# Kernel optimization log

Hardware: AMD Instinct MI355X
Metric: run time of the kernel (lower is better)

The kernel has to match this reference:

```python
import jax, jax.numpy as jnp
import numpy as np

# Model dims (match init_kwargs)
B, N, FIN, C, D, L, H = 16, 64, 16, 32, 4, 4, 8
EPS = 1e-6


def _sph(rhat):
    """Real spherical harmonics Y_l(rhat) for l=0..3. rhat: [...,3] unit vectors."""
    x, y, z = rhat[..., 0], rhat[..., 1], rhat[..., 2]
    Y0 = jnp.full(rhat.shape[:-1] + (1,), 0.5 * np.sqrt(1.0 / np.pi), rhat.dtype)
    c1 = np.sqrt(3.0 / (4.0 * np.pi))
    Y1 = c1 * jnp.stack([y, z, x], axis=-1)
    Y2 = jnp.stack([
        0.5 * np.sqrt(15 / np.pi) * x * y,
        0.5 * np.sqrt(15 / np.pi) * y * z,
        0.25 * np.sqrt(5 / np.pi) * (3 * z * z - 1.0),
        0.5 * np.sqrt(15 / np.pi) * x * z,
        0.25 * np.sqrt(15 / np.pi) * (x * x - y * y)], axis=-1)
    Y3 = jnp.stack([
        0.25 * np.sqrt(35 / (2 * np.pi)) * y * (3 * x * x - y * y),
        0.5 * np.sqrt(105 / np.pi) * x * y * z,
        0.25 * np.sqrt(21 / (2 * np.pi)) * y * (5 * z * z - 1.0),
        0.25 * np.sqrt(7 / np.pi) * z * (5 * z * z - 3.0),
        0.25 * np.sqrt(21 / (2 * np.pi)) * x * (5 * z * z - 1.0),
        0.25 * np.sqrt(105 / np.pi) * z * (x * x - y * y),
        0.25 * np.sqrt(35 / (2 * np.pi)) * x * (x * x - y * y)], axis=-1)
    return [Y0, Y1, Y2, Y3]


def _ln(v):
    mu = v.mean(-1, keepdims=True)
    var = ((v - mu) ** 2).mean(-1, keepdims=True)
    return (v - mu) * jax.lax.rsqrt(var + EPS)


def _forward(h, x, bond_type, Wemb, rw1, rb1, rw2, rb2, Wk, Wv, Wq, Wself, gnorm, bnorm, Wfinal, bfinal):
    Bq, Nq, _ = h.shape
    hd = C // H  # channels per head
    # Fully-connected graph: rel_pos[b, dst, src] = x_src - x_dst (matches xi[src]-xi[dst])
    rel = x[:, None, :, :] - x[:, :, None, :]
    dist = jnp.sqrt((rel * rel).sum(-1) + EPS)  # [B,N,N]
    rhat = rel / dist[..., None]
    Ys = _sph(rhat)
    # bond types -> one-hot(5) dropping class 0 -> 4 edge channels
    ef = jax.nn.one_hot(jnp.clip(bond_type, 0, 4), 5, dtype=h.dtype)[..., 1:]
    rin = jnp.concatenate([dist[..., None], ef], axis=-1)  # [B,N,N,5]
    eye = jnp.eye(Nq, dtype=bool)[None, :, :, None]  # mask self-edges
    # embed node feats to num_channels type-0; higher degrees start at zero
    f = [jnp.einsum('bnf,fc->bnc', h, Wemb)[..., None]] + \
        [jnp.zeros((Bq, Nq, C, 2 * l + 1), h.dtype) for l in range(1, D)]
    scale = 1.0 / np.sqrt(hd * sum(2 * l + 1 for l in range(D)))
    for li in range(L):
        # radial MLP with layer norm on (dist, edge_feat)
        hmid = jax.nn.relu(_ln(jnp.einsum('bdsi,ic->bdsc', rin, rw1[li]) + rb1[li]))
        r = (jnp.einsum('bdsc,co->bdso', hmid, rw2[li]) + rb2[li]).reshape(Bq, Nq, Nq, D, 4, C)
        logits = jnp.zeros((Bq, Nq, Nq, H), h.dtype)
        vs = []
        f0 = f[0][..., 0]  # [B,N,C]
        for l in range(D):
            M = 2 * l + 1
            # equivariant paths: (0->l) via Y_l lift, (l->l) identity
            sc_k = jnp.einsum('ci,bni->bnc', Wk[li, l, 0], f0)
            sc_v = jnp.einsum('ci,bni->bnc', Wv[li, l, 0], f0)
            id_k = jnp.einsum('ci,bnim->bncm', Wk[li, l, 1], f[l])
            id_v = jnp.einsum('ci,bnim->bncm', Wv[li, l, 1], f[l])
            Yl = Ys[l][:, :, :, None, :]  # [B,N,N,1,M]
            k = r[..., l, 0, :, None] * sc_k[:, None, :, :, None] * Yl + r[..., l, 1, :, None] * id_k[:, None]
            v = r[..., l, 2, :, None] * sc_v[:, None, :, :, None] * Yl + r[..., l, 3, :, None] * id_v[:, None]
            q = jnp.einsum('ci,bnim->bncm', Wq[li, l], f[l])  # dst-side query
            logits = logits + jnp.einsum('bdhcm,bdshcm->bdsh',
                                         q.reshape(Bq, Nq, H, hd, M),
                                         k.reshape(Bq, Nq, Nq, H, hd, M))
            vs.append(v)
        logits = jnp.where(eye, -1e9, logits * scale)
        attn = jax.nn.softmax(logits, axis=2)  # softmax over source nodes
        newf = []
        for l in range(D):
            M = 2 * l + 1
            o = jnp.einsum('bdsh,bdshcm->bdhcm', attn,
                           vs[l].reshape(Bq, Nq, Nq, H, hd, M)).reshape(Bq, Nq, C, M)
            o = o + jnp.einsum('ci,bnim->bncm', Wself[li, l], f[l])  # self-interaction skip
            # NormSE3: per-channel norm over the 2l+1 components, gated nonlinearity
            nrm = jnp.sqrt((o * o).sum(-1) + EPS)
            s = jax.nn.relu(gnorm[li, l] * nrm + bnorm[li, l])
            newf.append(o * (s / nrm)[..., None])
        f = newf
    # invariant readout: fiber_out = {0: D*C}; proj is Identity since D*C == d_gnn == 128
    inv = jnp.concatenate([f[0][..., 0]] + [jnp.sqrt((f[l] ** 2).sum(-1) + EPS) for l in range(1, D)], axis=-1)
    node_out = inv @ Wfinal + bfinal  # [B,N,128]
    return node_out.mean(axis=1)  # avg pooling -> [B,128]


def setup_inputs() -> dict:
    key = jax.random.key(0)
    ks = jax.random.split(key, 12)
    h = jax.random.normal(ks[0], (B, N, FIN), jnp.float32)
    x = 2.0 * jax.random.normal(ks[1], (B, N, 3), jnp.float32)
    bond_type = jax.random.randint(ks[2], (B, N, N), 0, 5)

    def init(k, shape, fan):
        return jax.random.normal(k, shape, jnp.float32) / np.sqrt(fan)

    return {
        'h': h, 'x': x, 'bond_type': bond_type,
        'Wemb': init(ks[3], (FIN, C), FIN),
        'rw1': init(ks[4], (L, 5, C), 5),
        'rb1': jnp.zeros((L, C), jnp.float32),
        'rw2': init(ks[5], (L, C, D * 4 * C), C),
        'rb2': jnp.zeros((L, D * 4 * C), jnp.float32),
        'Wk': init(ks[6], (L, D, 2, C, C), C),
        'Wv': init(ks[7], (L, D, 2, C, C), C),
        'Wq': init(ks[8], (L, D, C, C), C),
        'Wself': init(ks[9], (L, D, C, C), C),
        'gnorm': jnp.ones((L, D, C), jnp.float32),
        'bnorm': jnp.zeros((L, D, C), jnp.float32),
        'Wfinal': init(ks[10], (D * C, 128), D * C),
        'bfinal': jnp.zeros((128,), jnp.float32),
    }


def reference(h, x, bond_type, Wemb, rw1, rb1, rw2, rb2, Wk, Wv, Wq, Wself, gnorm, bnorm, Wfinal, bfinal):
    return _forward(h, x, bond_type, Wemb, rw1, rb1, rw2, rb2, Wk, Wv, Wq, Wself, gnorm, bnorm, Wfinal, bfinal)
```

## Files before the change

kernel.cpp:

```cpp
#include <hip/hip_runtime.h>
#include <hip/hip_bf16.h>


typedef float  f32x4  __attribute__((ext_vector_type(4)));
typedef short  bf16x8 __attribute__((ext_vector_type(8)));

__device__ __forceinline__ int lof(int mg)   { return (mg==0)?0:((mg<4)?1:((mg<9)?2:3)); }
__device__ __forceinline__ int mgb_of(int l) { return (l==0)?0:((l==1)?1:((l==2)?4:9)); }

__device__ __forceinline__ void nf_project2(const float* fl, float* out,
    const float* __restrict__ Wk, const float* __restrict__ Wv,
    const float* __restrict__ Wq, int li, int tid, int nT) {
  for (int o = tid; o < 2560; o += nT) {
    float acc = 0.f;
    if (o < 512) {
      int c = o >> 4, mg = o & 15, l = lof(mg);
      const float* w = Wq + (size_t)((li*4 + l)*32 + c) * 32;
      #pragma unroll
      for (int i = 0; i < 32; i++) acc += w[i] * fl[i*16 + mg];
    } else if (o < 1536) {
      int s = (o - 512) >> 1, kv = (o - 512) & 1;
      int c = s >> 4, mg = s & 15, l = lof(mg);
      const float* w = (kv ? Wv : Wk) + (size_t)(((li*4 + l)*2 + 1)*32 + c) * 32;
      #pragma unroll
      for (int i = 0; i < 32; i++) acc += w[i] * fl[i*16 + mg];
    } else {
      int s = (o - 1536) >> 1, kv = (o - 1536) & 1;
      int c = s >> 4, l = lof(s & 15);
      const float* w = (kv ? Wv : Wk) + (size_t)(((li*4 + l)*2 + 0)*32 + c) * 32;
      #pragma unroll
      for (int i = 0; i < 32; i++) acc += w[i] * fl[i*16];
    }
    out[o] = acc;
  }
}

__global__ __launch_bounds__(256) void prep_k(const float* __restrict__ h,
    const float* __restrict__ Wemb,
    const float* __restrict__ Wk, const float* __restrict__ Wv,
    const float* __restrict__ Wq,
    const float* __restrict__ rw2, const float* __restrict__ rb2,
    float* __restrict__ f, float* __restrict__ nf,
    __hip_bfloat16* __restrict__ rw2bh, __hip_bfloat16* __restrict__ rw2bl,
    float* __restrict__ rb2p) {
  __shared__ __align__(16) float fl[512];
  const int node = blockIdx.x;
  const int tid = threadIdx.x;

  const int gidx = blockIdx.x * 256 + tid;
  if (gidx < 65536) {
    int lli = gidx >> 14, rem = gidx & 16383;
    int np = rem >> 5, k = rem & 31;
    int c = np >> 4, l = (np >> 2) & 3, p = np & 3;
    float v = rw2[(size_t)lli*16384 + k*512 + l*128 + p*32 + c];
    __hip_bfloat16 hi = __float2bfloat16(v);
    __hip_bfloat16 lo = __float2bfloat16(v - __bfloat162float(hi));
    rw2bh[gidx] = hi;
    rw2bl[gidx] = lo;
  }
  if (gidx < 2048) {
    int lli = gidx >> 9, np = gidx & 511;
    int c = np >> 4, l = (np >> 2) & 3, p = np & 3;
    rb2p[gidx] = rb2[lli*512 + l*128 + p*32 + c];
  }

  fl[2*tid] = 0.f; fl[2*tid + 1] = 0.f;
  __syncthreads();
  if (tid < 32) {
    const float* hh = h + node * 16;
    float v = 0.f;
    #pragma unroll
    for (int i = 0; i < 16; i++) v += hh[i] * Wemb[i * 32 + tid];
    fl[tid * 16] = v;
  }
  __syncthreads();
  *reinterpret_cast<float2*>(f + (size_t)node * 512 + 2*tid) =
      *reinterpret_cast<const float2*>(fl + 2*tid);
  nf_project2(fl, nf + (size_t)node * 2560, Wk, Wv, Wq, 0, tid, 256);
}

__global__ __launch_bounds__(256) void attn_k(
    const float* __restrict__ f, const float* __restrict__ nf,
    float* __restrict__ fnext,
    const float* __restrict__ x, const int* __restrict__ bond,
    const float* __restrict__ rw1, const float* __restrict__ rb1,
    const __hip_bfloat16* __restrict__ rw2bh,
    const __hip_bfloat16* __restrict__ rw2bl,
    const float* __restrict__ rb2p,
    const float* __restrict__ Wself, const float* __restrict__ gnorm,
    const float* __restrict__ bnorm,
    const float* __restrict__ Wk, const float* __restrict__ Wv,
    const float* __restrict__ Wq,
    float* __restrict__ nf_out, int li) {
  __shared__ __align__(16) float Ysh[64][16];
  __shared__ float rinsh[64][8];
  __shared__ __align__(16) float fdst[512];
  __shared__ __align__(16) __hip_bfloat16 hmidb_hi[64][40];
  __shared__ __align__(16) __hip_bfloat16 hmidb_lo[64][40];
  __shared__ __align__(16) float rst[4][8*132];

  const int tid = threadIdx.x;
  const int bid = blockIdx.x;
  const int bd  = (bid & 7) * 128 + (bid >> 3);
  const int b = bd >> 6, d = bd & 63;
  const int wv = tid >> 6;
  const int t = tid & 63;

  const int slot0 = 128*wv + 2*t;
  const int oc  = slot0 >> 4;
  const int mg0 = slot0 & 15, mg1 = mg0 + 1;
  const int l0 = lof(mg0), l1 = lof(mg1);

  const int o0 = 2 * tid;
  *reinterpret_cast<float2*>(fdst + o0) =
      *reinterpret_cast<const float2*>(f + (size_t)bd * 512 + o0);
  const float2 qv = *reinterpret_cast<const float2*>(nf + (size_t)bd * 2560 + slot0);

  if (tid < 64) {
    const int s = tid;
    const float* xb = x + (size_t)b * 192;
    float xd = xb[d*3+0], yd = xb[d*3+1], zd = xb[d*3+2];
    float dx = xb[s*3+0] - xd, dy = xb[s*3+1] - yd, dz = xb[s*3+2] - zd;
    float dist = sqrtf(dx*dx + dy*dy + dz*dz + 1e-6f);
    float inv = 1.0f / dist;
    float xx = dx*inv, yy = dy*inv, zz = dz*inv;
    float* Y = Ysh[s];
    Y[0]  = 0.28209479177387814f;
    Y[1]  = 0.4886025119029199f * yy;
    Y[2]  = 0.4886025119029199f * zz;
    Y[3]  = 0.4886025119029199f * xx;
    Y[4]  = 1.0925484305920792f * xx * yy;
    Y[5]  = 1.0925484305920792f * yy * zz;
    Y[6]  = 0.31539156525252005f * (3.0f*zz*zz - 1.0f);
    Y[7]  = 1.0925484305920792f * xx * zz;
    Y[8]  = 0.5462742152960396f * (xx*xx - yy*yy);
    Y[9]  = 0.5900435899266435f * yy * (3.0f*xx*xx - yy*yy);
    Y[10] = 2.890611442640554f  * xx * yy * zz;
    Y[11] = 0.4570457994644658f * yy * (5.0f*zz*zz - 1.0f);
    Y[12] = 0.3731763325901154f * zz * (5.0f*zz*zz - 3.0f);
    Y[13] = 0.4570457994644658f * xx * (5.0f*zz*zz - 1.0f);
    Y[14] = 1.445305721320277f  * zz * (xx*xx - yy*yy);
    Y[15] = 0.5900435899266435f * xx * (xx*xx - yy*yy);
    rinsh[s][0] = dist;
    int bt = bond[(size_t)b * 4096 + d * 64 + s];
    bt = bt < 0 ? 0 : (bt > 4 ? 4 : bt);
    rinsh[s][1] = (bt == 1) ? 1.f : 0.f;
    rinsh[s][2] = (bt == 2) ? 1.f : 0.f;
    rinsh[s][3] = (bt == 3) ? 1.f : 0.f;
    rinsh[s][4] = (bt == 4) ? 1.f : 0.f;
  }

  const int ch = tid & 31;
  float w1r[5];
  #pragma unroll
  for (int i = 0; i < 5; i++) w1r[i] = rw1[(li*5 + i)*32 + ch];
  const float b1r = rb1[li*32 + ch];

  __syncthreads();

  #pragma unroll
  for (int p = 0; p < 8; p++) {
    const int e = p * 8 + (tid >> 5);
    float pre = b1r;
    #pragma unroll
    for (int i = 0; i < 5; i++) pre += rinsh[e][i] * w1r[i];
    float mu = pre;
    #pragma unroll
    for (int k = 16; k >= 1; k >>= 1) mu += __shfl_xor(mu, k, 32);
    mu *= 0.03125f;
    float dv = pre - mu;
    float var = dv * dv;
    #pragma unroll
    for (int k = 16; k >= 1; k >>= 1) var += __shfl_xor(var, k, 32);
    var *= 0.03125f;
    float hm = fmaxf(dv * rsqrtf(var + 1e-6f), 0.0f);
    __hip_bfloat16 hi = __float2bfloat16(hm);
    hmidb_hi[e][ch] = hi;
    hmidb_lo[e][ch] = __float2bfloat16(hm - __bfloat162float(hi));
  }
  __syncthreads();

  const int nfb = (b * 64) * 2560;
  const float4 bA = *reinterpret_cast<const float4*>(rb2p + li*512 + oc*16 + l0*4);
  const float4 bB = *reinterpret_cast<const float4*>(rb2p + li*512 + oc*16 + l1*4);
  const int rdA = (t >> 3)*16 + l0*4;
  const int rdB = (t >> 3)*16 + l1*4;
  const int afoff = li*16384 + (128*wv + (t & 15))*32 + (t >> 4)*8;
  const int bfrow = t & 7;
  const int bfk   = (t >> 4) * 8;
  const int myrow = t & 15;
  const int wcol  = (t >> 4)*4;
  float* rstw = &rst[wv][0];

  float m_run = -1e30f, l_run = 0.0f, acc0 = 0.0f, acc1 = 0.0f;

  auto consume4 = [&](int eg0, int rbase) {
    float4 kvv[4], svv[4];
    #pragma unroll
    for (int e2 = 0; e2 < 4; e2++) {
      const float* npp = nf + nfb + (eg0 + e2) * 2560;
      kvv[e2] = *reinterpret_cast<const float4*>(npp + 512 + 2*slot0);
      svv[e2] = *reinterpret_cast<const float4*>(npp + 1536 + 2*slot0);
    }
    float lg[4], vA[4], vB[4];
    #pragma unroll
    for (int e2 = 0; e2 < 4; e2++) {
      const int eg = eg0 + e2, row = rbase + e2;
      float4 rA = *reinterpret_cast<const float4*>(rstw + row*132 + rdA);
      float4 rB = *reinterpret_cast<const float4*>(rstw + row*132 + rdB);
      rA.x += bA.x; rA.y += bA.y; rA.z += bA.z; rA.w += bA.w;
      rB.x += bB.x; rB.y += bB.y; rB.z += bB.z; rB.w += bB.w;
      const float ym0 = Ysh[eg][mg0], ym1 = Ysh[eg][mg1];
      const float k0 = rA.x * svv[e2].x * ym0 + rA.y * kvv[e2].x;
      const float k1 = rB.x * svv[e2].z * ym1 + rB.y * kvv[e2].z;
      float pl = qv.x * k0 + qv.y * k1;
      pl += __shfl_xor(pl, 1);
      pl += __shfl_xor(pl, 2);
      pl += __shfl_xor(pl, 4);
      pl += __shfl_xor(pl, 8);
      pl += __shfl_xor(pl, 16);
      lg[e2] = (eg == d) ? -1e9f : pl * 0.125f;
      vA[e2] = rA.z * svv[e2].y * ym0 + rA.w * kvv[e2].y;
      vB[e2] = rB.z * svv[e2].w * ym1 + rB.w * kvv[e2].w;
    }
    const float m4 = fmaxf(fmaxf(lg[0], lg[1]), fmaxf(lg[2], lg[3]));
    const float m_new = fmaxf(m_run, m4);
    const float resc = __expf(m_run - m_new);
    acc0 *= resc; acc1 *= resc; l_run *= resc;
    #pragma unroll
    for (int e2 = 0; e2 < 4; e2++) {
      const float wgt = __expf(lg[e2] - m_new);
      l_run += wgt;
      acc0 += wgt * vA[e2];
      acc1 += wgt * vB[e2];
    }
    m_run = m_new;
  };

  for (int mt8 = 0; mt8 < 8; mt8++) {
    const int e0 = mt8 * 8;
    const bf16x8 bhi = *reinterpret_cast<const bf16x8*>(&hmidb_hi[e0 + bfrow][bfk]);
    const bf16x8 blo = *reinterpret_cast<const bf16x8*>(&hmidb_lo[e0 + bfrow][bfk]);
    #pragma unroll
    for (int ct = 0; ct < 8; ct++) {
      const bf16x8 ah = *reinterpret_cast<const bf16x8*>(
          reinterpret_cast<const short*>(rw2bh) + afoff + ct*512);
      const bf16x8 al = *reinterpret_cast<const bf16x8*>(
          reinterpret_cast<const short*>(rw2bl) + afoff + ct*512);
      f32x4 c = {0.f, 0.f, 0.f, 0.f};
      c = __builtin_amdgcn_mfma_f32_16x16x32_bf16(al, bhi, c, 0, 0, 0);
      c = __builtin_amdgcn_mfma_f32_16x16x32_bf16(ah, blo, c, 0, 0, 0);
      c = __builtin_amdgcn_mfma_f32_16x16x32_bf16(ah, bhi, c, 0, 0, 0);
      if (myrow < 8)
        *reinterpret_cast<f32x4*>(rstw + myrow*132 + ct*16 + wcol) = c;
    }
    asm volatile("s_waitcnt lgkmcnt(0)" ::: "memory");
    __builtin_amdgcn_sched_barrier(0);
    consume4(e0,     0);
    consume4(e0 + 4, 4);
  }

  const float invl = 1.0f / l_run;
  acc0 *= invl; acc1 *= invl;
  {
    const float* w0 = Wself + (size_t)((li*4 + l0)*32 + oc) * 32;
    const float* w1 = Wself + (size_t)((li*4 + l1)*32 + oc) * 32;
    #pragma unroll
    for (int i = 0; i < 32; i++) {
      acc0 += w0[i] * fdst[i*16 + mg0];
      acc1 += w1[i] * fdst[i*16 + mg1];
    }
  }
  __syncthreads();
  float* osh = &Ysh[0][0];
  osh[slot0] = acc0; osh[slot0 + 1] = acc1;
  __syncthreads();
  float* facsh = &rinsh[0][0];
  if (tid < 128) {
    const int c2 = tid >> 2, l2 = tid & 3;
    const int mb = mgb_of(l2), M2 = 2*l2 + 1;
    float ss = 0.f;
    for (int m = 0; m < M2; m++) { float v = osh[c2*16 + mb + m]; ss += v*v; }
    const float nrm = sqrtf(ss + 1e-6f);
    const float gg = gnorm[(li*4 + l2)*32 + c2];
    const float bb = bnorm[(li*4 + l2)*32 + c2];
    const float sg = fmaxf(gg*nrm + bb, 0.f);
    facsh[c2*4 + l2] = sg / nrm;
  }
  __syncthreads();
  const float g0 = acc0 * facsh[oc*4 + l0];
  const float g1 = acc1 * facsh[oc*4 + l1];
  *reinterpret_cast<float2*>(fnext + (size_t)bd * 512 + slot0) = make_float2(g0, g1);

  if (nf_out) {
    osh[slot0] = g0; osh[slot0 + 1] = g1;
    __syncthreads();
    nf_project2(osh, nf_out + (size_t)bd * 2560, Wk, Wv, Wq, li + 1, tid, 256);
  }
}

__global__ __launch_bounds__(256) void readout_k(const float* __restrict__ f,
    const float* __restrict__ Wfinal, const float* __restrict__ bfinal,
    float* __restrict__ out) {
  __shared__ float invs[2][128];
  __shared__ float inv1[128];
  const int b = blockIdx.x;
  const int tid = threadIdx.x;
  const int j = tid & 127, half = tid >> 7;
  float p = 0.f;
  for (int n = half*32; n < half*32 + 32; n++) {
    const float* fn = f + (size_t)(b*64 + n) * 512;
    float v;
    if (j < 32) {
      v = fn[j*16];
    } else {
      int l = j >> 5, c = j & 31;
      int mb = mgb_of(l), M = 2*l + 1;
      float ss = 0.f;
      for (int m = 0; m < M; m++) { float t = fn[c*16 + mb + m]; ss += t*t; }
      v = sqrtf(ss + 1e-6f);
    }
    p += v;
  }
  invs[half][j] = p;
  __syncthreads();
  if (tid < 128) inv1[tid] = (invs[0][tid] + invs[1][tid]) * (1.0f / 64.0f);
  __syncthreads();
  if (tid < 128) {
    float acc = bfinal[tid];
    for (int k = 0; k < 128; k++) acc += inv1[k] * Wfinal[k*128 + tid];
    out[b*128 + tid] = acc;
  }
}

extern "C" void kernel_launch(void* const* d_in, const int* in_sizes, int n_in,
                              void* d_out, int out_size, void* d_ws, size_t ws_size,
                              hipStream_t stream) {
  (void)in_sizes; (void)n_in; (void)out_size; (void)ws_size;
  const float* h      = (const float*)d_in[0];
  const float* x      = (const float*)d_in[1];
  const int*   bond   = (const int*)d_in[2];
  const float* Wemb   = (const float*)d_in[3];
  const float* rw1    = (const float*)d_in[4];
  const float* rb1    = (const float*)d_in[5];
  const float* rw2    = (const float*)d_in[6];
  const float* rb2    = (const float*)d_in[7];
  const float* Wk     = (const float*)d_in[8];
  const float* Wv     = (const float*)d_in[9];
  const float* Wq     = (const float*)d_in[10];
  const float* Wself  = (const float*)d_in[11];
  const float* gnorm  = (const float*)d_in[12];
  const float* bnorm  = (const float*)d_in[13];
  const float* Wfinal = (const float*)d_in[14];
  const float* bfinal = (const float*)d_in[15];
  float* out = (float*)d_out;

  float* ws  = (float*)d_ws;
  float* fA   = ws;
  float* fB   = fA + 524288;
  float* nfA  = fB + 524288;
  float* nfB  = nfA + 2621440;
  float* rb2p = nfB + 2621440;
  __hip_bfloat16* rw2bh = (__hip_bfloat16*)(rb2p + 2048);
  __hip_bfloat16* rw2bl = (__hip_bfloat16*)(rb2p + 2048 + 32768);

  prep_k<<<1024, 256, 0, stream>>>(h, Wemb, Wk, Wv, Wq, rw2, rb2,
                                   fA, nfA, rw2bh, rw2bl, rb2p);

  float* fc = fA;  float* fn2 = fB;
  float* nfc = nfA; float* nfn = nfB;
  for (int li = 0; li < 4; li++) {
    attn_k<<<1024, 256, 0, stream>>>(fc, nfc, fn2, x, bond,
                                     rw1, rb1, rw2bh, rw2bl, rb2p,
                                     Wself, gnorm, bnorm, Wk, Wv, Wq,
                                     (li < 3) ? nfn : nullptr, li);
    float* t = fc; fc = fn2; fn2 = t;
    t = nfc; nfc = nfn; nfn = t;
  }

  readout_k<<<16, 256, 0, stream>>>(fc, Wfinal, bfinal, out);
}
```

Before: 412.8 us.

## Prefetch neighbor K/V loads, coalesce rw2 repack reads, split readout across nodes

The attention loop now double-buffers the per-neighbor nf loads, issuing the next group of four before the math on the current group so global latency overlaps with compute. The rw2 bf16 split in prep_k is changed to read coalesced and scatter its writes instead. The readout is split into a per-node kernel over 1024 blocks that writes invariants to a scratch buffer, then a small reduction-and-linear kernel. This adds a launch and extra registers for the prefetch buffers in exchange for more latency hiding and parallelism.

```diff
diff --git a/kernel.cpp b/kernel.cpp
--- a/kernel.cpp
+++ b/kernel.cpp
@@ -50,18 +50,19 @@
   const int gidx = blockIdx.x * 256 + tid;
   if (gidx < 65536) {
     int lli = gidx >> 14, rem = gidx & 16383;
-    int np = rem >> 5, k = rem & 31;
-    int c = np >> 4, l = (np >> 2) & 3, p = np & 3;
-    float v = rw2[(size_t)lli*16384 + k*512 + l*128 + p*32 + c];
+    int k = rem >> 9, col = rem & 511;
+    int l = col >> 7, p = (col >> 5) & 3, c = col & 31;
+    int np = c*16 + l*4 + p;
+    float v = rw2[gidx];
     __hip_bfloat16 hi = __float2bfloat16(v);
     __hip_bfloat16 lo = __float2bfloat16(v - __bfloat162float(hi));
-    rw2bh[gidx] = hi;
-    rw2bl[gidx] = lo;
+    rw2bh[lli*16384 + np*32 + k] = hi;
+    rw2bl[lli*16384 + np*32 + k] = lo;
   }
   if (gidx < 2048) {
-    int lli = gidx >> 9, np = gidx & 511;
-    int c = np >> 4, l = (np >> 2) & 3, p = np & 3;
-    rb2p[gidx] = rb2[lli*512 + l*128 + p*32 + c];
+    int lli = gidx >> 9, col = gidx & 511;
+    int l = col >> 7, p = (col >> 5) & 3, c = col & 31;
+    rb2p[lli*512 + c*16 + l*4 + p] = rb2[gidx];
   }
 
   fl[2*tid] = 0.f; fl[2*tid + 1] = 0.f;
@@ -194,14 +195,15 @@
 
   float m_run = -1e30f, l_run = 0.0f, acc0 = 0.0f, acc1 = 0.0f;
 
-  auto consume4 = [&](int eg0, int rbase) {
-    float4 kvv[4], svv[4];
+  auto load4 = [&](int eg0, float4* kv, float4* sv) {
     #pragma unroll
     for (int e2 = 0; e2 < 4; e2++) {
       const float* npp = nf + nfb + (eg0 + e2) * 2560;
-      kvv[e2] = *reinterpret_cast<const float4*>(npp + 512 + 2*slot0);
-      svv[e2] = *reinterpret_cast<const float4*>(npp + 1536 + 2*slot0);
-    }
+      kv[e2] = *reinterpret_cast<const float4*>(npp + 512 + 2*slot0);
+      sv[e2] = *reinterpret_cast<const float4*>(npp + 1536 + 2*slot0);
+    }
+  };
+  auto math4 = [&](int eg0, int rbase, const float4* kv, const float4* sv) {
     float lg[4], vA[4], vB[4];
     #pragma unroll
     for (int e2 = 0; e2 < 4; e2++) {
@@ -211,8 +213,8 @@
       rA.x += bA.x; rA.y += bA.y; rA.z += bA.z; rA.w += bA.w;
       rB.x += bB.x; rB.y += bB.y; rB.z += bB.z; rB.w += bB.w;
       const float ym0 = Ysh[eg][mg0], ym1 = Ysh[eg][mg1];
-      const float k0 = rA.x * svv[e2].x * ym0 + rA.y * kvv[e2].x;
-      const float k1 = rB.x * svv[e2].z * ym1 + rB.y * kvv[e2].z;
+      const float k0 = rA.x * sv[e2].x * ym0 + rA.y * kv[e2].x;
+      const float k1 = rB.x * sv[e2].z * ym1 + rB.y * kv[e2].z;
       float pl = qv.x * k0 + qv.y * k1;
       pl += __shfl_xor(pl, 1);
       pl += __shfl_xor(pl, 2);
@@ -220,8 +222,8 @@
       pl += __shfl_xor(pl, 8);
       pl += __shfl_xor(pl, 16);
       lg[e2] = (eg == d) ? -1e9f : pl * 0.125f;
-      vA[e2] = rA.z * svv[e2].y * ym0 + rA.w * kvv[e2].y;
-      vB[e2] = rB.z * svv[e2].w * ym1 + rB.w * kvv[e2].w;
+      vA[e2] = rA.z * sv[e2].y * ym0 + rA.w * kv[e2].y;
+      vB[e2] = rB.z * sv[e2].w * ym1 + rB.w * kv[e2].w;
     }
     const float m4 = fmaxf(fmaxf(lg[0], lg[1]), fmaxf(lg[2], lg[3]));
     const float m_new = fmaxf(m_run, m4);
@@ -237,6 +239,8 @@
     m_run = m_new;
   };
 
+  float4 kA[4], sA[4], kB[4], sB[4];
+  load4(0, kA, sA);
   for (int mt8 = 0; mt8 < 8; mt8++) {
     const int e0 = mt8 * 8;
     const bf16x8 bhi = *reinterpret_cast<const bf16x8*>(&hmidb_hi[e0 + bfrow][bfk]);
@@ -256,8 +260,10 @@
     }
     asm volatile("s_waitcnt lgkmcnt(0)" ::: "memory");
     __builtin_amdgcn_sched_barrier(0);
-    consume4(e0,     0);
-    consume4(e0 + 4, 4);
+    load4(e0 + 4, kB, sB);
+    math4(e0, 0, kA, sA);
+    if (mt8 < 7) load4(e0 + 8, kA, sA);
+    math4(e0 + 4, 4, kB, sB);
   }
 
   const float invl = 1.0f / l_run;
@@ -299,38 +305,38 @@
   }
 }
 
-__global__ __launch_bounds__(256) void readout_k(const float* __restrict__ f,
+__global__ __launch_bounds__(128) void readout1_k(const float* __restrict__ f,
+    float* __restrict__ invbuf) {
+  const int node = blockIdx.x;
+  const int j = threadIdx.x;
+  const float* fn = f + (size_t)node * 512;
+  float v;
+  if (j < 32) {
+    v = fn[j*16];
+  } else {
+    int l = j >> 5, c = j & 31;
+    int mb = mgb_of(l), M = 2*l + 1;
+    float ss = 0.f;
+    for (int m = 0; m < M; m++) { float t2 = fn[c*16 + mb + m]; ss += t2*t2; }
+    v = sqrtf(ss + 1e-6f);
+  }
+  invbuf[(size_t)node * 128 + j] = v;
+}
+
+__global__ __launch_bounds__(128) void readout2_k(const float* __restrict__ invbuf,
     const float* __restrict__ Wfinal, const float* __restrict__ bfinal,
     float* __restrict__ out) {
-  __shared__ float invs[2][128];
   __shared__ float inv1[128];
   const int b = blockIdx.x;
   const int tid = threadIdx.x;
-  const int j = tid & 127, half = tid >> 7;
   float p = 0.f;
-  for (int n = half*32; n < half*32 + 32; n++) {
-    const float* fn = f + (size_t)(b*64 + n) * 512;
-    float v;
-    if (j < 32) {
-      v = fn[j*16];
-    } else {
-      int l = j >> 5, c = j & 31;
-      int mb = mgb_of(l), M = 2*l + 1;
-      float ss = 0.f;
-      for (int m = 0; m < M; m++) { float t = fn[c*16 + mb + m]; ss += t*t; }
-      v = sqrtf(ss + 1e-6f);
-    }
-    p += v;
-  }
-  invs[half][j] = p;
-  __syncthreads();
-  if (tid < 128) inv1[tid] = (invs[0][tid] + invs[1][tid]) * (1.0f / 64.0f);
-  __syncthreads();
-  if (tid < 128) {
-    float acc = bfinal[tid];
-    for (int k = 0; k < 128; k++) acc += inv1[k] * Wfinal[k*128 + tid];
-    out[b*128 + tid] = acc;
-  }
+  for (int n = 0; n < 64; n++)
+    p += invbuf[(size_t)(b*64 + n) * 128 + tid];
+  inv1[tid] = p * (1.0f / 64.0f);
+  __syncthreads();
+  float acc = bfinal[tid];
+  for (int k = 0; k < 128; k++) acc += inv1[k] * Wfinal[k*128 + tid];
+  out[b*128 + tid] = acc;
 }
 
 extern "C" void kernel_launch(void* const* d_in, const int* in_sizes, int n_in,
@@ -378,5 +384,7 @@
     t = nfc; nfc = nfn; nfn = t;
   }
 
-  readout_k<<<16, 256, 0, stream>>>(fc, Wfinal, bfinal, out);
-}
+  float* invbuf = nfn;
+  readout1_k<<<1024, 128, 0, stream>>>(fc, invbuf);
+  readout2_k<<<16, 128, 0, stream>>>(invbuf, Wfinal, bfinal, out);
+}
```

Measured after the change: 381.5 us. 7.6% less time.
